# Kernel optimization log

Measured on AMD Instinct MI355X. Metric: run time of the kernel, lower is better.

The kernel has to match this reference:

```python
import jax, jax.numpy as jnp
import numpy as np

T, B, N, H, NT = 4096, 8, 256, 512, 5
W_SCALE = 0.02


def setup_inputs() -> dict:
    key = jax.random.key(0)
    ks = jax.random.split(key, 32)
    f32 = jnp.float32
    d = {}
    d['v_action'] = jax.random.normal(ks[0], (N, B, H), f32)
    d['v_frame'] = jax.random.normal(ks[1], (T, B, H), f32)
    d['v_task'] = jax.random.normal(ks[2], (NT, B, H), f32)
    d['v_mask'] = jax.random.randint(ks[3], (B, N), 0, 2, jnp.int32).at[:, 0].set(1)
    d['t_action'] = jax.random.normal(ks[4], (N, B, H), f32)
    d['t_frame'] = jax.random.normal(ks[5], (T, B, H), f32)
    d['t_task'] = jax.random.normal(ks[6], (NT, B, H), f32)
    d['t_mask'] = jax.random.randint(ks[7], (B, N), 0, 2, jnp.int32).at[:, 0].set(1)
    names = ['v_Wq', 'v_Wk', 'v_Wv', 'v_Wo', 't_Wq', 't_Wk', 't_Wv', 't_Wo']
    for i, nm in enumerate(names):
        d[nm] = jax.random.normal(ks[8 + i], (H, H), f32) * W_SCALE
    d['v_aw'] = jnp.asarray(0.1, f32)
    d['t_aw'] = jnp.asarray(0.1, f32)
    d['v_tw'] = jax.random.normal(ks[20], (H, 1), f32) * W_SCALE
    d['v_tb'] = jnp.zeros((1,), f32)
    d['t_tw'] = jax.random.normal(ks[21], (H, 1), f32) * W_SCALE
    d['t_tb'] = jnp.zeros((1,), f32)
    return d


def _compute_logit(frame, action, Wq, Wk):
    # frame: [T,B,H] queries, action: [N,B,H] keys -> logits [B,T,N]
    q = jnp.einsum('tbf,fh->tbh', frame, Wq)
    k = jnp.einsum('nba,ah->nbh', action, Wk)
    return jnp.einsum('tbh,nbh->btn', q, k) / jnp.sqrt(jnp.asarray(q.shape[-1], q.dtype))


def _compute_output(logit, alignment, action, frame, mask, Wv, Wo, aw):
    # shared detached cross-domain alignment, gated by sigmoid(alignment_weight)
    combined = logit + jax.nn.sigmoid(aw) * alignment          # [B,T,N]
    nomask = combined
    masked = jnp.where(mask[:, None, :] > 0, combined, -jnp.inf)
    attn = jax.nn.softmax(masked, axis=-1)                      # softmax over protos N
    v = jnp.einsum('nba,af->nbf', action, Wv)                   # values from protos
    out = jnp.einsum('btn,nbf->tbf', attn, v)
    out = jnp.einsum('tbf,fg->tbg', out, Wo) + frame            # residual to frames
    return out, nomask


def reference(v_action, v_frame, v_task, v_mask, t_action, t_frame, t_task, t_mask,
              v_Wq, v_Wk, v_Wv, v_Wo, v_aw, v_tw, v_tb,
              t_Wq, t_Wk, t_Wv, t_Wo, t_aw, t_tw, t_tb):
    v_logit = _compute_logit(v_frame, v_action, v_Wq, v_Wk)
    t_logit = _compute_logit(t_frame, t_action, t_Wq, t_Wk)
    v_share = jax.lax.stop_gradient(v_logit)
    t_share = jax.lax.stop_gradient(t_logit)
    v_out, v_nm = _compute_output(v_logit, t_share, v_action, v_frame, v_mask, v_Wv, v_Wo, v_aw)
    t_out, t_nm = _compute_output(t_logit, v_share, t_action, t_frame, t_mask, t_Wv, t_Wo, t_aw)
    v_ta = jnp.einsum('kbh,ho->kbo', v_task, v_tw) + v_tb       # [ntask,B,1]
    t_ta = jnp.einsum('kbh,ho->kbo', t_task, t_tw) + t_tb
    return (v_out, t_out,
            jnp.transpose(v_nm, (0, 2, 1)),                      # [B,N,T]
            jnp.transpose(t_nm, (0, 2, 1)),
            v_ta, t_ta)
```

## Files before the change

kernel.cpp:

```cpp
#include <hip/hip_runtime.h>
#include <hip/hip_bf16.h>
#include <cstddef>
#include <cstdint>

#define T_DIM 4096
#define B_DIM 8
#define N_DIM 256
#define H_DIM 512
#define NT_DIM 5

typedef __attribute__((ext_vector_type(8))) short short8;
typedef __attribute__((ext_vector_type(4))) float f32x4;

__device__ __forceinline__ short cvt_bf16(float f) {
  __hip_bfloat16 h = __float2bfloat16(f);
  union { __hip_bfloat16 h; short s; } u; u.h = h; return u.s;
}
__device__ __forceinline__ float bf2f(short s) {
  union { uint32_t u; float f; } v; v.u = ((uint32_t)(uint16_t)s) << 16;
  return v.f;
}

typedef __attribute__((address_space(1))) const void gvoid_t;
typedef __attribute__((address_space(3))) void lvoid_t;
__device__ __forceinline__ void gl_lds16(const void* g, void* lds_wave_base) {
  __builtin_amdgcn_global_load_lds((gvoid_t*)(uintptr_t)g,
                                   (lvoid_t*)(uint32_t)(uintptr_t)lds_wave_base,
                                   16, 0, 0);
}

struct GP {
  const void* A[2];
  const short* B[2];
  void* C[2];
  const float* R[2];
};

template<typename TA, typename TC, bool ADD_RES>
__global__ __launch_bounds__(256)
void gemm_tn(GP p, int zlog, long long a_bs, int lda,
             long long b_bs, int ldb, long long c_bs, int ldc,
             int K, float scale) {
  constexpr bool F32A = (sizeof(TA) == 4);
  constexpr int ASTR = F32A ? 40 : 32;
  constexpr int AB = 128 * ASTR * 2;
  constexpr int BB = 128 * 32 * 2;
  constexpr int HALF = AB + BB;
  constexpr int EPIB = 4 * 16 * 68 * 4;
  constexpr int SMEMB = (2 * HALF) > EPIB ? (2 * HALF) : EPIB;
  __shared__ __align__(16) char smem[SMEMB];

  const int tid  = threadIdx.x;
  const int lane = tid & 63;
  const int wave = tid >> 6;
  const int wr   = (wave >> 1) * 64;
  const int wc   = (wave & 1) * 64;
  const int lrow = lane & 15;
  const int kgrp = lane >> 4;

  const int dom = blockIdx.z >> zlog;
  const long long zz = blockIdx.z & ((1u << zlog) - 1u);

  const TA*    Abase = (const TA*)p.A[dom] + zz * a_bs + (long long)(blockIdx.x * 128) * lda;
  const short* Bbase = p.B[dom] + zz * b_bs + (long long)(blockIdx.y * 128) * ldb;

  const int ch_r  = lane >> 2;
  const int swcol = ((lane & 3) ^ (ch_r & 3)) * 8;
  const int srow = tid >> 1;
  const int scol = (tid & 1) * 16;

  f32x4 acc[4][4] = {};
  f32x4 pv[4];

  auto stageA_bf16 = [&](int bufoff, int k0) {
    short* As = (short*)(smem + bufoff);
    #pragma unroll
    for (int i = 0; i < 2; ++i) {
      const int c = wave + 4 * i;
      gl_lds16((const short*)Abase + (long long)(c * 16 + ch_r) * lda + k0 + swcol,
               &As[c * 512]);
    }
  };
  auto stageB = [&](int bufoff, int k0) {
    short* Bs = (short*)(smem + bufoff + AB);
    #pragma unroll
    for (int i = 0; i < 2; ++i) {
      const int c = wave + 4 * i;
      gl_lds16(Bbase + (long long)(c * 16 + ch_r) * ldb + k0 + swcol, &Bs[c * 512]);
    }
  };
  auto loadA_f32 = [&](int k0) {
    const float* gp = (const float*)Abase + (long long)srow * lda + k0 + scol;
    pv[0] = *(const f32x4*)(gp + 0);
    pv[1] = *(const f32x4*)(gp + 4);
    pv[2] = *(const f32x4*)(gp + 8);
    pv[3] = *(const f32x4*)(gp + 12);
  };
  auto writeA_f32 = [&](int bufoff) {
    short* As = (short*)(smem + bufoff);
    short8 s0, s1;
    #pragma unroll
    for (int e = 0; e < 4; ++e) {
      s0[e]     = cvt_bf16(pv[0][e]);
      s0[4 + e] = cvt_bf16(pv[1][e]);
      s1[e]     = cvt_bf16(pv[2][e]);
      s1[4 + e] = cvt_bf16(pv[3][e]);
    }
    *(short8*)&As[srow * ASTR + scol]     = s0;
    *(short8*)&As[srow * ASTR + scol + 8] = s1;
  };
  auto compute = [&](int bufoff) {
    short* As = (short*)(smem + bufoff);
    short* Bs = (short*)(smem + bufoff + AB);
    short8 af[4], bfr[4];
    const int u = kgrp ^ (lrow & 3);
    #pragma unroll
    for (int i = 0; i < 4; ++i) {
      const int row = wr + i * 16 + lrow;
      if constexpr (F32A) af[i] = *(const short8*)&As[row * ASTR + kgrp * 8];
      else                af[i] = *(const short8*)&As[row * 32 + u * 8];
    }
    #pragma unroll
    for (int j = 0; j < 4; ++j) {
      const int row = wc + j * 16 + lrow;
      bfr[j] = *(const short8*)&Bs[row * 32 + u * 8];
    }
    #pragma unroll
    for (int i = 0; i < 4; ++i)
      #pragma unroll
      for (int j = 0; j < 4; ++j)
        acc[i][j] = __builtin_amdgcn_mfma_f32_16x16x32_bf16(af[i], bfr[j], acc[i][j], 0, 0, 0);
  };

  const int NT = K >> 5;
  if constexpr (F32A) {
    loadA_f32(0); writeA_f32(0); stageB(0, 0);
    __syncthreads();
    int cur = 0;
    for (int t = 0; t < NT; ++t) {
      const int nxt = (cur ^ 1) * HALF;
      const bool more = (t + 1 < NT);
      if (more) { loadA_f32((t + 1) << 5); stageB(nxt, (t + 1) << 5); }
      compute(cur * HALF);
      if (more) writeA_f32(nxt);
      __syncthreads();
      cur ^= 1;
    }
  } else {
    stageA_bf16(0, 0); stageB(0, 0);
    for (int t = 0; t < NT; ++t) {
      const int cb_ = (t & 1) * HALF;
      const int nb_ = ((t + 1) & 1) * HALF;
      __builtin_amdgcn_s_barrier();
      if (t + 1 < NT) { stageA_bf16(nb_, (t + 1) << 5); stageB(nb_, (t + 1) << 5); }
      __builtin_amdgcn_sched_barrier(0);
      if (t + 1 < NT) asm volatile("s_waitcnt vmcnt(4)" ::: "memory");
      else            asm volatile("s_waitcnt vmcnt(0)" ::: "memory");
      __builtin_amdgcn_sched_barrier(0);
      __builtin_amdgcn_s_barrier();
      __builtin_amdgcn_sched_barrier(0);
      compute(cb_);
    }
  }

  __syncthreads();
  float* myEp = (float*)smem + wave * (16 * 68);
  TC* Cd = (TC*)p.C[dom];
  const float* Res = p.R[dom];
  const long long cb = zz * c_bs;
  const int gm = blockIdx.x * 128 + wr;
  const int gn = blockIdx.y * 128 + wc;
  const int er = lane >> 2;
  const int ec = (lane & 3) * 16;

  f32x4 resA[4], resB[4];
  if constexpr (ADD_RES) {
    const long long b0 = cb + (long long)(gm + er) * ldc + gn + ec;
    #pragma unroll
    for (int q = 0; q < 4; ++q) resA[q] = *(const f32x4*)&Res[b0 + q * 4];
  }

  #pragma unroll
  for (int i = 0; i < 4; ++i) {
    if constexpr (ADD_RES) {
      if (i < 3) {
        const long long bn = cb + (long long)(gm + (i + 1) * 16 + er) * ldc + gn + ec;
        #pragma unroll
        for (int q = 0; q < 4; ++q) resB[q] = *(const f32x4*)&Res[bn + q * 4];
      }
    }
    #pragma unroll
    for (int j = 0; j < 4; ++j)
      #pragma unroll
      for (int r = 0; r < 4; ++r)
        myEp[(kgrp * 4 + r) * 68 + j * 16 + lrow] = acc[i][j][r];
    float vals[16];
    #pragma unroll
    for (int q = 0; q < 4; ++q) {
      f32x4 t4 = *(const f32x4*)&myEp[er * 68 + ec + q * 4];
      vals[q * 4 + 0] = t4[0]; vals[q * 4 + 1] = t4[1];
      vals[q * 4 + 2] = t4[2]; vals[q * 4 + 3] = t4[3];
    }
    const int row_g = gm + i * 16 + er;
    const long long base = cb + (long long)row_g * ldc + gn + ec;
    if constexpr (sizeof(TC) == 2) {
      short8 s0, s1;
      #pragma unroll
      for (int e = 0; e < 8; ++e) {
        s0[e] = cvt_bf16(vals[e] * scale);
        s1[e] = cvt_bf16(vals[8 + e] * scale);
      }
      *(short8*)&Cd[base]     = s0;
      *(short8*)&Cd[base + 8] = s1;
    } else {
      #pragma unroll
      for (int q = 0; q < 4; ++q) {
        f32x4 o;
        #pragma unroll
        for (int e = 0; e < 4; ++e) o[e] = vals[q * 4 + e] * scale;
        if constexpr (ADD_RES) {
          #pragma unroll
          for (int e = 0; e < 4; ++e) o[e] += resA[q][e];
        }
        *(f32x4*)&Cd[base + q * 4] = o;
      }
    }
    if constexpr (ADD_RES) {
      #pragma unroll
      for (int q = 0; q < 4; ++q) resA[q] = resB[q];
    }
  }
}

struct WSrc { const float* p[8]; };

__global__ __launch_bounds__(256)
void wtrans_kernel(WSrc s, short* __restrict__ dst) {
  __shared__ float tile[32][33];
  const int w = blockIdx.z;
  const float* src = s.p[w];
  short* d = dst + (long long)w * H_DIM * H_DIM;
  const int tx = threadIdx.x, ty = threadIdx.y;
  const int n0 = blockIdx.x * 32, k0 = blockIdx.y * 32;
  #pragma unroll
  for (int i = 0; i < 4; ++i)
    tile[ty + 8 * i][tx] = src[(long long)(k0 + ty + 8 * i) * H_DIM + n0 + tx];
  __syncthreads();
  #pragma unroll
  for (int i = 0; i < 4; ++i)
    d[(long long)(n0 + ty + 8 * i) * H_DIM + k0 + tx] = cvt_bf16(tile[tx][ty + 8 * i]);
}

__global__ __launch_bounds__(256)
void softmax_fused(const short* __restrict__ Lv, const short* __restrict__ Lt,
                   const int* __restrict__ vmask, const int* __restrict__ tmask,
                   const float* __restrict__ vaw, const float* __restrict__ taw,
                   short* __restrict__ Av, short* __restrict__ At,
                   float* __restrict__ Onm_v, float* __restrict__ Onm_t) {
  __shared__ float tile[16 * 260];
  __shared__ int msk[2][256];
  const int tid = threadIdx.x;
  const int b = blockIdx.y, t0 = blockIdx.x * 16;
  const int r = tid >> 4, seg = tid & 15;
  msk[0][tid] = vmask[b * 256 + tid];
  msk[1][tid] = tmask[b * 256 + tid];
  __syncthreads();
  const float sv = 1.f / (1.f + __expf(-vaw[0]));
  const float st = 1.f / (1.f + __expf(-taw[0]));
  const long long off = ((long long)b * T_DIM + t0 + r) * N_DIM + seg * 16;

  short8 lv0 = *(const short8*)&Lv[off];
  short8 lv1 = *(const short8*)&Lv[off + 8];
  short8 lt0 = *(const short8*)&Lt[off];
  short8 lt1 = *(const short8*)&Lt[off + 8];
  float cv[16], ct[16];
  #pragma unroll
  for (int i = 0; i < 8; ++i) {
    float a0 = bf2f(lv0[i]), b0 = bf2f(lt0[i]);
    float a1 = bf2f(lv1[i]), b1 = bf2f(lt1[i]);
    cv[i]     = a0 + sv * b0;  ct[i]     = b0 + st * a0;
    cv[8 + i] = a1 + sv * b1;  ct[8 + i] = b1 + st * a1;
  }

#define EMIT_DOMAIN(CVAL, DI, AOUT, ONM) do {                                   \
    const int4 mA = *(const int4*)&msk[DI][seg * 16 + 0];                       \
    const int4 mB = *(const int4*)&msk[DI][seg * 16 + 4];                       \
    const int4 mC = *(const int4*)&msk[DI][seg * 16 + 8];                       \
    const int4 mD = *(const int4*)&msk[DI][seg * 16 + 12];                      \
    const int mk[16] = {mA.x, mA.y, mA.z, mA.w, mB.x, mB.y, mB.z, mB.w,         \
                        mC.x, mC.y, mC.z, mC.w, mD.x, mD.y, mD.z, mD.w};        \
    float mx = -3.4e38f;                                                        \
    _Pragma("unroll")                                                           \
    for (int q = 0; q < 16; ++q) if (mk[q] > 0) mx = fmaxf(mx, CVAL[q]);        \
    _Pragma("unroll")                                                           \
    for (int sh = 1; sh < 16; sh <<= 1) mx = fmaxf(mx, __shfl_xor(mx, sh));     \
    float ev[16]; float ssum = 0.f;                                             \
    _Pragma("unroll")                                                           \
    for (int q = 0; q < 16; ++q) {                                              \
      ev[q] = (mk[q] > 0) ? __expf(CVAL[q] - mx) : 0.f; ssum += ev[q];          \
    }                                                                           \
    _Pragma("unroll")                                                           \
    for (int sh = 1; sh < 16; sh <<= 1) ssum += __shfl_xor(ssum, sh);           \
    const float inv = 1.f / ssum;                                               \
    short8 o0, o1;                                                              \
    _Pragma("unroll")                                                           \
    for (int q = 0; q < 8; ++q) {                                               \
      o0[q] = cvt_bf16(ev[q] * inv); o1[q] = cvt_bf16(ev[8 + q] * inv);         \
    }                                                                           \
    *(short8*)&AOUT[off] = o0; *(short8*)&AOUT[off + 8] = o1;                   \
    _Pragma("unroll")                                                           \
    for (int q = 0; q < 4; ++q) {                                               \
      f32x4 tv; tv[0] = CVAL[q * 4]; tv[1] = CVAL[q * 4 + 1];                   \
      tv[2] = CVAL[q * 4 + 2]; tv[3] = CVAL[q * 4 + 3];                         \
      *(f32x4*)&tile[r * 260 + seg * 16 + q * 4] = tv;                          \
    }                                                                           \
    __syncthreads();                                                            \
    {                                                                           \
      float* obase = &ONM[((long long)b * N_DIM + tid) * T_DIM + t0];           \
      _Pragma("unroll")                                                         \
      for (int g = 0; g < 4; ++g) {                                             \
        f32x4 wv;                                                               \
        wv[0] = tile[(4 * g + 0) * 260 + tid];                                  \
        wv[1] = tile[(4 * g + 1) * 260 + tid];                                  \
        wv[2] = tile[(4 * g + 2) * 260 + tid];                                  \
        wv[3] = tile[(4 * g + 3) * 260 + tid];                                  \
        *(f32x4*)&obase[4 * g] = wv;                                            \
      }                                                                         \
    }                                                                           \
    __syncthreads();                                                            \
  } while (0)

  EMIT_DOMAIN(cv, 0, Av, Onm_v);
  EMIT_DOMAIN(ct, 1, At, Onm_t);
#undef EMIT_DOMAIN
}

__global__ __launch_bounds__(1024)
void task_kernel(const float* __restrict__ vtask, const float* __restrict__ ttask,
                 const float* __restrict__ vtw, const float* __restrict__ vtb,
                 const float* __restrict__ ttw, const float* __restrict__ ttb,
                 float* __restrict__ out_v, float* __restrict__ out_t) {
  const int wave = threadIdx.x >> 6;
  const int lane = threadIdx.x & 63;
  const int dom = wave >> 3;
  const int b   = wave & 7;
  const float* task = dom ? ttask : vtask;
  const float* tw   = dom ? ttw : vtw;
  const float  tb   = (dom ? ttb : vtb)[0];
  float* o = dom ? out_t : out_v;
  for (int k = 0; k < NT_DIM; ++k) {
    const float* row = task + ((long long)k * B_DIM + b) * H_DIM;
    float s = 0.f;
    for (int c = lane; c < H_DIM; c += 64) s += row[c] * tw[c];
    #pragma unroll
    for (int d = 32; d > 0; d >>= 1) s += __shfl_xor(s, d);
    if (lane == 0) o[k * B_DIM + b] = s + tb;
  }
}

extern "C" void kernel_launch(void* const* d_in, const int* in_sizes, int n_in,
                              void* d_out, int out_size, void* d_ws, size_t ws_size,
                              hipStream_t stream) {
  const float* v_action = (const float*)d_in[0];
  const float* v_frame  = (const float*)d_in[1];
  const float* v_task   = (const float*)d_in[2];
  const int*   v_mask   = (const int*)d_in[3];
  const float* t_action = (const float*)d_in[4];
  const float* t_frame  = (const float*)d_in[5];
  const float* t_task   = (const float*)d_in[6];
  const int*   t_mask   = (const int*)d_in[7];
  const float* v_aw = (const float*)d_in[16];
  const float* t_aw = (const float*)d_in[17];
  const float* v_tw = (const float*)d_in[18];
  const float* v_tb = (const float*)d_in[19];
  const float* t_tw = (const float*)d_in[20];
  const float* t_tb = (const float*)d_in[21];

  const long long TBH = (long long)T_DIM * B_DIM * H_DIM;
  const long long BTN = (long long)B_DIM * T_DIM * N_DIM;
  const long long NBH = (long long)N_DIM * B_DIM * H_DIM;
  const long long WS  = (long long)H_DIM * H_DIM;

  float* out = (float*)d_out;
  float* out_v   = out;
  float* out_t   = out + TBH;
  float* out_vnm = out + 2 * TBH;
  float* out_tnm = out + 2 * TBH + BTN;
  float* out_vta = out + 2 * TBH + 2 * BTN;
  float* out_tta = out_vta + NT_DIM * B_DIM;

  char* w = (char*)d_ws;
  auto alloc = [&](long long bytes) {
    char* p = w; w += (bytes + 255) & ~255LL; return p;
  };
  short* WT   = (short*)alloc(8 * WS * 2);
  short* Qv   = (short*)alloc(TBH * 2);
  short* Qt   = (short*)alloc(TBH * 2);
  short* KVv  = (short*)alloc(2048LL * 1024 * 2);
  short* KVt  = (short*)alloc(2048LL * 1024 * 2);
  short* VWTv = (short*)alloc(NBH * 2);
  short* VWTt = (short*)alloc(NBH * 2);
  short* Av   = (short*)alloc(BTN * 2);
  short* At   = (short*)alloc(BTN * 2);
  short* Lv   = (short*)alloc(BTN * 2);
  short* Lt   = (short*)alloc(BTN * 2);

  const float rsq = 0.044194173824159216f;

  WSrc ws8;
  for (int i = 0; i < 8; ++i) ws8.p[i] = (const float*)d_in[8 + i];
  wtrans_kernel<<<dim3(16, 16, 8), dim3(32, 8), 0, stream>>>(ws8, WT);

  {
    GP p = {{v_frame, t_frame}, {WT + 0 * WS, WT + 4 * WS}, {Qv, Qt}, {nullptr, nullptr}};
    gemm_tn<float, short, false><<<dim3(256, 4, 2), dim3(256), 0, stream>>>(
        p, 0, 0LL, H_DIM, 0LL, H_DIM, 0LL, H_DIM, 512, 1.f);
  }

  {
    GP p = {{v_action, t_action}, {WT + 1 * WS, WT + 5 * WS}, {KVv, KVt}, {nullptr, nullptr}};
    gemm_tn<float, short, false><<<dim3(16, 8, 2), dim3(256), 0, stream>>>(
        p, 0, 0LL, H_DIM, 0LL, H_DIM, 0LL, 1024, 512, 1.f);
  }

  {
    GP p = {{WT + 3 * WS, WT + 7 * WS}, {KVv + 512, KVt + 512}, {VWTv, VWTt},
            {nullptr, nullptr}};
    gemm_tn<short, short, false><<<dim3(4, 2, 16), dim3(256), 0, stream>>>(
        p, 3, 0LL, H_DIM, 1024LL, 8192, (long long)H_DIM * N_DIM, N_DIM, 512, 1.f);
  }

  {
    GP p = {{Qv, Qt}, {KVv, KVt}, {Lv, Lt}, {nullptr, nullptr}};
    gemm_tn<short, short, false><<<dim3(32, 2, 16), dim3(256), 0, stream>>>(
        p, 3, 512LL, B_DIM * H_DIM, 1024LL, 8192,
        (long long)T_DIM * N_DIM, N_DIM, 512, rsq);
  }

  softmax_fused<<<dim3(T_DIM / 16, B_DIM), dim3(256), 0, stream>>>(
      Lv, Lt, v_mask, t_mask, v_aw, t_aw, Av, At, out_vnm, out_tnm);

  {
    GP p = {{Av, At}, {VWTv, VWTt}, {out_v, out_t}, {v_frame, t_frame}};
    gemm_tn<short, float, true><<<dim3(32, 4, 16), dim3(256), 0, stream>>>(
        p, 3, (long long)T_DIM * N_DIM, N_DIM, (long long)H_DIM * N_DIM, N_DIM,
        512LL, B_DIM * H_DIM, 256, 1.f);
  }

  task_kernel<<<dim3(1), dim3(1024), 0, stream>>>(
      v_task, t_task, v_tw, v_tb, t_tw, t_tb, out_vta, out_tta);
}
```

Before: 292.3 us.

## Fuse logits GEMM with cross-domain softmax and triple-buffer bf16 GEMM loads

The QK logits GEMM for both domains now runs inside a new kernel that keeps logits in registers, mixes them across domains, applies the masked softmax, and writes the bf16 attention weights and the fp32 transposed logits directly. This removes the bf16 logits round-trip through global memory and one kernel launch. It also keeps the logits in fp32 before mixing instead of rounding them to bf16. Separately, the bf16 path of the generic GEMM moves from double to triple buffering with a deeper prefetch distance. The cost is a large LDS footprint (144KB per block) and many block-wide syncs in the epilogue, which limits occupancy.

```diff
diff --git a/kernel.cpp b/kernel.cpp
--- a/kernel.cpp
+++ b/kernel.cpp
@@ -15,10 +15,6 @@
 __device__ __forceinline__ short cvt_bf16(float f) {
   __hip_bfloat16 h = __float2bfloat16(f);
   union { __hip_bfloat16 h; short s; } u; u.h = h; return u.s;
-}
-__device__ __forceinline__ float bf2f(short s) {
-  union { uint32_t u; float f; } v; v.u = ((uint32_t)(uint16_t)s) << 16;
-  return v.f;
 }
 
 typedef __attribute__((address_space(1))) const void gvoid_t;
@@ -28,6 +24,8 @@
                                    (lvoid_t*)(uint32_t)(uintptr_t)lds_wave_base,
                                    16, 0, 0);
 }
+
+#define MFMA16(a, b, c) __builtin_amdgcn_mfma_f32_16x16x32_bf16(a, b, c, 0, 0, 0)
 
 struct GP {
   const void* A[2];
@@ -46,8 +44,9 @@
   constexpr int AB = 128 * ASTR * 2;
   constexpr int BB = 128 * 32 * 2;
   constexpr int HALF = AB + BB;
+  constexpr int NBUF = F32A ? 2 : 3;
   constexpr int EPIB = 4 * 16 * 68 * 4;
-  constexpr int SMEMB = (2 * HALF) > EPIB ? (2 * HALF) : EPIB;
+  constexpr int SMEMB = (NBUF * HALF) > EPIB ? (NBUF * HALF) : EPIB;
   __shared__ __align__(16) char smem[SMEMB];
 
   const int tid  = threadIdx.x;
@@ -129,7 +128,7 @@
     for (int i = 0; i < 4; ++i)
       #pragma unroll
       for (int j = 0; j < 4; ++j)
-        acc[i][j] = __builtin_amdgcn_mfma_f32_16x16x32_bf16(af[i], bfr[j], acc[i][j], 0, 0, 0);
+        acc[i][j] = MFMA16(af[i], bfr[j], acc[i][j]);
   };
 
   const int NT = K >> 5;
@@ -148,14 +147,20 @@
     }
   } else {
     stageA_bf16(0, 0); stageB(0, 0);
+    stageA_bf16(HALF, 32); stageB(HALF, 32);
     for (int t = 0; t < NT; ++t) {
-      const int cb_ = (t & 1) * HALF;
-      const int nb_ = ((t + 1) & 1) * HALF;
+      const int cb_ = (t % 3) * HALF;
       __builtin_amdgcn_s_barrier();
-      if (t + 1 < NT) { stageA_bf16(nb_, (t + 1) << 5); stageB(nb_, (t + 1) << 5); }
-      __builtin_amdgcn_sched_barrier(0);
-      if (t + 1 < NT) asm volatile("s_waitcnt vmcnt(4)" ::: "memory");
-      else            asm volatile("s_waitcnt vmcnt(0)" ::: "memory");
+      if (t + 2 < NT) {
+        const int nb_ = ((t + 2) % 3) * HALF;
+        stageA_bf16(nb_, (t + 2) << 5); stageB(nb_, (t + 2) << 5);
+        __builtin_amdgcn_sched_barrier(0);
+        asm volatile("s_waitcnt vmcnt(8)" ::: "memory");
+      } else if (t + 1 < NT) {
+        asm volatile("s_waitcnt vmcnt(4)" ::: "memory");
+      } else {
+        asm volatile("s_waitcnt vmcnt(0)" ::: "memory");
+      }
       __builtin_amdgcn_sched_barrier(0);
       __builtin_amdgcn_s_barrier();
       __builtin_amdgcn_sched_barrier(0);
@@ -230,6 +235,201 @@
       for (int q = 0; q < 4; ++q) resA[q] = resB[q];
     }
   }
+}
+
+__global__ __launch_bounds__(512)
+void logits_softmax_fused(const short* __restrict__ Qvg, const short* __restrict__ Qtg,
+                          const short* __restrict__ KVv, const short* __restrict__ KVt,
+                          const int* __restrict__ vmask, const int* __restrict__ tmask,
+                          const float* __restrict__ vaw, const float* __restrict__ taw,
+                          short* __restrict__ Avg, short* __restrict__ Atg,
+                          float* __restrict__ Onm_v, float* __restrict__ Onm_t) {
+  constexpr int TILEB = 48 * 1024;
+  __shared__ __align__(16) char smem[3 * TILEB];
+  __shared__ float rowstat[128][4];
+
+  const int tid  = threadIdx.x;
+  const int lane = tid & 63;
+  const int wave = tid >> 6;
+  const int wm   = wave >> 2;
+  const int wn   = wave & 3;
+  const int lrow = lane & 15;
+  const int kgrp = lane >> 4;
+  const int b    = blockIdx.y;
+  const int t0   = blockIdx.x * 128;
+
+  const float sv = 1.f / (1.f + __expf(-vaw[0]));
+  const float st = 1.f / (1.f + __expf(-taw[0]));
+  const float rsq = 0.044194173824159216f;
+
+  int mkv[4], mkt[4];
+  #pragma unroll
+  for (int j = 0; j < 4; ++j) {
+    const int n = wn * 64 + j * 16 + lrow;
+    mkv[j] = vmask[b * 256 + n];
+    mkt[j] = tmask[b * 256 + n];
+  }
+
+  const int ch_r = lane >> 2;
+  const int sw8  = ((lane & 3) ^ (ch_r & 3)) * 8;
+  const short* gsrc[6];
+  int loff[6];
+  #pragma unroll
+  for (int i = 0; i < 6; ++i) {
+    const int c = wave * 6 + i;
+    const short* s;
+    if (c < 8)       s = Qvg + (long long)(t0 + c * 16 + ch_r) * 4096 + b * 512;
+    else if (c < 16) s = Qtg + (long long)(t0 + (c - 8) * 16 + ch_r) * 4096 + b * 512;
+    else if (c < 32) s = KVv + (long long)((c - 16) * 16 + ch_r) * 8192 + b * 1024;
+    else             s = KVt + (long long)((c - 32) * 16 + ch_r) * 8192 + b * 1024;
+    gsrc[i] = s + sw8;
+    loff[i] = c * 1024;
+  }
+  auto stage = [&](int buf, int k0) {
+    #pragma unroll
+    for (int i = 0; i < 6; ++i)
+      gl_lds16(gsrc[i] + k0, smem + buf * TILEB + loff[i]);
+  };
+
+  f32x4 accv[4][4] = {}, acct[4][4] = {};
+
+  auto compute = [&](int buf) {
+    const short* L = (const short*)(smem + buf * TILEB);
+    const int u = kgrp ^ (lrow & 3);
+    short8 qv[4], qt[4], kv[4], kt[4];
+    #pragma unroll
+    for (int i = 0; i < 4; ++i) {
+      const int r = wm * 64 + i * 16 + lrow;
+      qv[i] = *(const short8*)&L[r * 32 + u * 8];
+      qt[i] = *(const short8*)&L[4096 + r * 32 + u * 8];
+    }
+    #pragma unroll
+    for (int j = 0; j < 4; ++j) {
+      const int r = wn * 64 + j * 16 + lrow;
+      kv[j] = *(const short8*)&L[8192 + r * 32 + u * 8];
+      kt[j] = *(const short8*)&L[16384 + r * 32 + u * 8];
+    }
+    #pragma unroll
+    for (int i = 0; i < 4; ++i)
+      #pragma unroll
+      for (int j = 0; j < 4; ++j) {
+        accv[i][j] = MFMA16(qv[i], kv[j], accv[i][j]);
+        acct[i][j] = MFMA16(qt[i], kt[j], acct[i][j]);
+      }
+  };
+
+  stage(0, 0); stage(1, 32);
+  #pragma unroll 1
+  for (int t = 0; t < 16; ++t) {
+    __builtin_amdgcn_s_barrier();
+    if (t + 2 < 16) {
+      stage((t + 2) % 3, (t + 2) * 32);
+      __builtin_amdgcn_sched_barrier(0);
+      asm volatile("s_waitcnt vmcnt(12)" ::: "memory");
+    } else if (t + 1 < 16) {
+      asm volatile("s_waitcnt vmcnt(6)" ::: "memory");
+    } else {
+      asm volatile("s_waitcnt vmcnt(0)" ::: "memory");
+    }
+    __builtin_amdgcn_sched_barrier(0);
+    __builtin_amdgcn_s_barrier();
+    __builtin_amdgcn_sched_barrier(0);
+    compute(t % 3);
+  }
+  __syncthreads();
+
+  #pragma unroll
+  for (int i = 0; i < 4; ++i)
+    #pragma unroll
+    for (int j = 0; j < 4; ++j) {
+      f32x4 a = accv[i][j], c = acct[i][j];
+      #pragma unroll
+      for (int e = 0; e < 4; ++e) {
+        accv[i][j][e] = rsq * (a[e] + sv * c[e]);
+        acct[i][j][e] = rsq * (c[e] + st * a[e]);
+      }
+    }
+
+#define DOM_OUT(ACC, MK, AV_G, ONM_G) do {                                          \
+    float lm[4][4];                                                                 \
+    _Pragma("unroll") for (int i = 0; i < 4; ++i)                                   \
+    _Pragma("unroll") for (int r = 0; r < 4; ++r) {                                 \
+      float m = -3.4e38f;                                                           \
+      _Pragma("unroll") for (int j = 0; j < 4; ++j)                                 \
+        if (MK[j] > 0) m = fmaxf(m, ACC[i][j][r]);                                  \
+      m = fmaxf(m, __shfl_xor(m, 1)); m = fmaxf(m, __shfl_xor(m, 2));               \
+      m = fmaxf(m, __shfl_xor(m, 4)); m = fmaxf(m, __shfl_xor(m, 8));               \
+      lm[i][r] = m;                                                                 \
+    }                                                                               \
+    if (lrow == 0) {                                                                \
+      _Pragma("unroll") for (int i = 0; i < 4; ++i)                                 \
+      _Pragma("unroll") for (int r = 0; r < 4; ++r)                                 \
+        rowstat[wm * 64 + i * 16 + kgrp * 4 + r][wn] = lm[i][r];                    \
+    }                                                                               \
+    __syncthreads();                                                                \
+    _Pragma("unroll") for (int i = 0; i < 4; ++i)                                   \
+    _Pragma("unroll") for (int r = 0; r < 4; ++r) {                                 \
+      f32x4 s = *(const f32x4*)&rowstat[wm * 64 + i * 16 + kgrp * 4 + r][0];        \
+      lm[i][r] = fmaxf(fmaxf(s[0], s[1]), fmaxf(s[2], s[3]));                       \
+    }                                                                               \
+    __syncthreads();                                                                \
+    float ls[4][4];                                                                 \
+    _Pragma("unroll") for (int i = 0; i < 4; ++i)                                   \
+    _Pragma("unroll") for (int r = 0; r < 4; ++r) {                                 \
+      float s = 0.f;                                                                \
+      _Pragma("unroll") for (int j = 0; j < 4; ++j)                                 \
+        if (MK[j] > 0) s += __expf(ACC[i][j][r] - lm[i][r]);                        \
+      s += __shfl_xor(s, 1); s += __shfl_xor(s, 2);                                 \
+      s += __shfl_xor(s, 4); s += __shfl_xor(s, 8);                                 \
+      ls[i][r] = s;                                                                 \
+    }                                                                               \
+    if (lrow == 0) {                                                                \
+      _Pragma("unroll") for (int i = 0; i < 4; ++i)                                 \
+      _Pragma("unroll") for (int r = 0; r < 4; ++r)                                 \
+        rowstat[wm * 64 + i * 16 + kgrp * 4 + r][wn] = ls[i][r];                    \
+    }                                                                               \
+    __syncthreads();                                                                \
+    _Pragma("unroll") for (int i = 0; i < 4; ++i)                                   \
+    _Pragma("unroll") for (int r = 0; r < 4; ++r) {                                 \
+      f32x4 s = *(const f32x4*)&rowstat[wm * 64 + i * 16 + kgrp * 4 + r][0];        \
+      ls[i][r] = 1.f / (s[0] + s[1] + s[2] + s[3]);                                 \
+    }                                                                               \
+    __syncthreads();                                                                \
+    {                    \
+      short* AL = (short*)smem;                                                     \
+      _Pragma("unroll") for (int i = 0; i < 4; ++i)                                 \
+      _Pragma("unroll") for (int j = 0; j < 4; ++j)                                 \
+      _Pragma("unroll") for (int r = 0; r < 4; ++r) {                               \
+        float e = (MK[j] > 0) ? __expf(ACC[i][j][r] - lm[i][r]) * ls[i][r] : 0.f;   \
+        AL[(wm * 64 + i * 16 + kgrp * 4 + r) * 264 + wn * 64 + j * 16 + lrow] =     \
+            cvt_bf16(e);                                                            \
+      }                                                                             \
+      __syncthreads();                                                              \
+      const int rr = tid >> 2, cb0 = (tid & 3) * 64;                                \
+      short* dst = AV_G + ((long long)b * T_DIM + t0 + rr) * 256 + cb0;             \
+      _Pragma("unroll") for (int q = 0; q < 8; ++q)                                 \
+        *(short8*)&dst[q * 8] = *(const short8*)&AL[rr * 264 + cb0 + q * 8];        \
+      __syncthreads();                                                              \
+    }                                                                               \
+    {                \
+      float* OL = (float*)smem;                                                     \
+      _Pragma("unroll") for (int i = 0; i < 4; ++i)                                 \
+      _Pragma("unroll") for (int j = 0; j < 4; ++j)                                 \
+      _Pragma("unroll") for (int r = 0; r < 4; ++r)                                 \
+        OL[(wn * 64 + j * 16 + lrow) * 132 + wm * 64 + i * 16 + kgrp * 4 + r] =     \
+            ACC[i][j][r];                                                           \
+      __syncthreads();                                                              \
+      const int nn = tid >> 1, c0 = (tid & 1) * 64;                                 \
+      float* dst = ONM_G + ((long long)b * 256 + nn) * T_DIM + t0 + c0;             \
+      _Pragma("unroll") for (int q = 0; q < 16; ++q)                                \
+        *(f32x4*)&dst[q * 4] = *(const f32x4*)&OL[nn * 132 + c0 + q * 4];           \
+      __syncthreads();                                                              \
+    }                                                                               \
+  } while (0)
+
+  DOM_OUT(accv, mkv, Avg, Onm_v);
+  DOM_OUT(acct, mkt, Atg, Onm_t);
+#undef DOM_OUT
 }
 
 struct WSrc { const float* p[8]; };
@@ -249,90 +449,6 @@
   #pragma unroll
   for (int i = 0; i < 4; ++i)
     d[(long long)(n0 + ty + 8 * i) * H_DIM + k0 + tx] = cvt_bf16(tile[tx][ty + 8 * i]);
-}
-
-__global__ __launch_bounds__(256)
-void softmax_fused(const short* __restrict__ Lv, const short* __restrict__ Lt,
-                   const int* __restrict__ vmask, const int* __restrict__ tmask,
-                   const float* __restrict__ vaw, const float* __restrict__ taw,
-                   short* __restrict__ Av, short* __restrict__ At,
-                   float* __restrict__ Onm_v, float* __restrict__ Onm_t) {
-  __shared__ float tile[16 * 260];
-  __shared__ int msk[2][256];
-  const int tid = threadIdx.x;
-  const int b = blockIdx.y, t0 = blockIdx.x * 16;
-  const int r = tid >> 4, seg = tid & 15;
-  msk[0][tid] = vmask[b * 256 + tid];
-  msk[1][tid] = tmask[b * 256 + tid];
-  __syncthreads();
-  const float sv = 1.f / (1.f + __expf(-vaw[0]));
-  const float st = 1.f / (1.f + __expf(-taw[0]));
-  const long long off = ((long long)b * T_DIM + t0 + r) * N_DIM + seg * 16;
-
-  short8 lv0 = *(const short8*)&Lv[off];
-  short8 lv1 = *(const short8*)&Lv[off + 8];
-  short8 lt0 = *(const short8*)&Lt[off];
-  short8 lt1 = *(const short8*)&Lt[off + 8];
-  float cv[16], ct[16];
-  #pragma unroll
-  for (int i = 0; i < 8; ++i) {
-    float a0 = bf2f(lv0[i]), b0 = bf2f(lt0[i]);
-    float a1 = bf2f(lv1[i]), b1 = bf2f(lt1[i]);
-    cv[i]     = a0 + sv * b0;  ct[i]     = b0 + st * a0;
-    cv[8 + i] = a1 + sv * b1;  ct[8 + i] = b1 + st * a1;
-  }
-
-#define EMIT_DOMAIN(CVAL, DI, AOUT, ONM) do {                                   \
-    const int4 mA = *(const int4*)&msk[DI][seg * 16 + 0];                       \
-    const int4 mB = *(const int4*)&msk[DI][seg * 16 + 4];                       \
-    const int4 mC = *(const int4*)&msk[DI][seg * 16 + 8];                       \
-    const int4 mD = *(const int4*)&msk[DI][seg * 16 + 12];                      \
-    const int mk[16] = {mA.x, mA.y, mA.z, mA.w, mB.x, mB.y, mB.z, mB.w,         \
-                        mC.x, mC.y, mC.z, mC.w, mD.x, mD.y, mD.z, mD.w};        \
-    float mx = -3.4e38f;                                                        \
-    _Pragma("unroll")                                                           \
-    for (int q = 0; q < 16; ++q) if (mk[q] > 0) mx = fmaxf(mx, CVAL[q]);        \
-    _Pragma("unroll")                                                           \
-    for (int sh = 1; sh < 16; sh <<= 1) mx = fmaxf(mx, __shfl_xor(mx, sh));     \
-    float ev[16]; float ssum = 0.f;                                             \
-    _Pragma("unroll")                                                           \
-    for (int q = 0; q < 16; ++q) {                                              \
-      ev[q] = (mk[q] > 0) ? __expf(CVAL[q] - mx) : 0.f; ssum += ev[q];          \
-    }                                                                           \
-    _Pragma("unroll")                                                           \
-    for (int sh = 1; sh < 16; sh <<= 1) ssum += __shfl_xor(ssum, sh);           \
-    const float inv = 1.f / ssum;                                               \
-    short8 o0, o1;                                                              \
-    _Pragma("unroll")                                                           \
-    for (int q = 0; q < 8; ++q) {                                               \
-      o0[q] = cvt_bf16(ev[q] * inv); o1[q] = cvt_bf16(ev[8 + q] * inv);         \
-    }                                                                           \
-    *(short8*)&AOUT[off] = o0; *(short8*)&AOUT[off + 8] = o1;                   \
-    _Pragma("unroll")                                                           \
-    for (int q = 0; q < 4; ++q) {                                               \
-      f32x4 tv; tv[0] = CVAL[q * 4]; tv[1] = CVAL[q * 4 + 1];                   \
-      tv[2] = CVAL[q * 4 + 2]; tv[3] = CVAL[q * 4 + 3];                         \
-      *(f32x4*)&tile[r * 260 + seg * 16 + q * 4] = tv;                          \
-    }                                                                           \
-    __syncthreads();                                                            \
-    {                                                                           \
-      float* obase = &ONM[((long long)b * N_DIM + tid) * T_DIM + t0];           \
-      _Pragma("unroll")                                                         \
-      for (int g = 0; g < 4; ++g) {                                             \
-        f32x4 wv;                                                               \
-        wv[0] = tile[(4 * g + 0) * 260 + tid];                                  \
-        wv[1] = tile[(4 * g + 1) * 260 + tid];                                  \
-        wv[2] = tile[(4 * g + 2) * 260 + tid];                                  \
-        wv[3] = tile[(4 * g + 3) * 260 + tid];                                  \
-        *(f32x4*)&obase[4 * g] = wv;                                            \
-      }                                                                         \
-    }                                                                           \
-    __syncthreads();                                                            \
-  } while (0)
-
-  EMIT_DOMAIN(cv, 0, Av, Onm_v);
-  EMIT_DOMAIN(ct, 1, At, Onm_t);
-#undef EMIT_DOMAIN
 }
 
 __global__ __launch_bounds__(1024)
@@ -402,10 +518,6 @@
   short* VWTt = (short*)alloc(NBH * 2);
   short* Av   = (short*)alloc(BTN * 2);
   short* At   = (short*)alloc(BTN * 2);
-  short* Lv   = (short*)alloc(BTN * 2);
-  short* Lt   = (short*)alloc(BTN * 2);
-
-  const float rsq = 0.044194173824159216f;
 
   WSrc ws8;
   for (int i = 0; i < 8; ++i) ws8.p[i] = (const float*)d_in[8 + i];
@@ -430,15 +542,8 @@
         p, 3, 0LL, H_DIM, 1024LL, 8192, (long long)H_DIM * N_DIM, N_DIM, 512, 1.f);
   }
 
-  {
-    GP p = {{Qv, Qt}, {KVv, KVt}, {Lv, Lt}, {nullptr, nullptr}};
-    gemm_tn<short, short, false><<<dim3(32, 2, 16), dim3(256), 0, stream>>>(
-        p, 3, 512LL, B_DIM * H_DIM, 1024LL, 8192,
-        (long long)T_DIM * N_DIM, N_DIM, 512, rsq);
-  }
-
-  softmax_fused<<<dim3(T_DIM / 16, B_DIM), dim3(256), 0, stream>>>(
-      Lv, Lt, v_mask, t_mask, v_aw, t_aw, Av, At, out_vnm, out_tnm);
+  logits_softmax_fused<<<dim3(T_DIM / 128, B_DIM), dim3(512), 0, stream>>>(
+      Qv, Qt, KVv, KVt, v_mask, t_mask, v_aw, t_aw, Av, At, out_vnm, out_tnm);
 
   {
     GP p = {{Av, At}, {VWTv, VWTt}, {out_v, out_t}, {v_frame, t_frame}};
```

Result: slower. 312.8 us (+7.0%).

## Deepen GEMM K-loop pipeline to triple-buffered LDS with prefetch distance two

Applied to the files above, without the earlier changes.

Both GEMM variants now keep three LDS stages so async global-to-LDS loads run two K-tiles ahead of compute, with explicit vmcnt waits sized to the extra loads in flight. The f32-A path keeps A double-buffered through registers but triple-buffers B, and replaces __syncthreads with manual waitcnt and barrier pairs. The aim is to hide global memory latency better in the K loop. In exchange the kernel uses more LDS, which can lower occupancy, and hand-tuned vmcnt counts risk subtle ordering bugs.

```diff
diff --git a/kernel.cpp b/kernel.cpp
--- a/kernel.cpp
+++ b/kernel.cpp
@@ -28,6 +28,8 @@
                                    (lvoid_t*)(uint32_t)(uintptr_t)lds_wave_base,
                                    16, 0, 0);
 }
+
+#define MFMA16(a, b, c) __builtin_amdgcn_mfma_f32_16x16x32_bf16(a, b, c, 0, 0, 0)
 
 struct GP {
   const void* A[2];
@@ -47,7 +49,8 @@
   constexpr int BB = 128 * 32 * 2;
   constexpr int HALF = AB + BB;
   constexpr int EPIB = 4 * 16 * 68 * 4;
-  constexpr int SMEMB = (2 * HALF) > EPIB ? (2 * HALF) : EPIB;
+  constexpr int BODYB = F32A ? (2 * AB + 3 * BB) : (3 * HALF);
+  constexpr int SMEMB = BODYB > EPIB ? BODYB : EPIB;
   __shared__ __align__(16) char smem[SMEMB];
 
   const int tid  = threadIdx.x;
@@ -72,8 +75,8 @@
   f32x4 acc[4][4] = {};
   f32x4 pv[4];
 
-  auto stageA_bf16 = [&](int bufoff, int k0) {
-    short* As = (short*)(smem + bufoff);
+  auto stageA_bf16 = [&](int buf, int k0) {
+    short* As = (short*)(smem + buf * HALF);
     #pragma unroll
     for (int i = 0; i < 2; ++i) {
       const int c = wave + 4 * i;
@@ -81,8 +84,16 @@
                &As[c * 512]);
     }
   };
-  auto stageB = [&](int bufoff, int k0) {
-    short* Bs = (short*)(smem + bufoff + AB);
+  auto stageB_bf16 = [&](int buf, int k0) {
+    short* Bs = (short*)(smem + buf * HALF + AB);
+    #pragma unroll
+    for (int i = 0; i < 2; ++i) {
+      const int c = wave + 4 * i;
+      gl_lds16(Bbase + (long long)(c * 16 + ch_r) * ldb + k0 + swcol, &Bs[c * 512]);
+    }
+  };
+  auto stageB_f32p = [&](int buf, int k0) {
+    short* Bs = (short*)(smem + 2 * AB + buf * BB);
     #pragma unroll
     for (int i = 0; i < 2; ++i) {
       const int c = wave + 4 * i;
@@ -96,8 +107,8 @@
     pv[2] = *(const f32x4*)(gp + 8);
     pv[3] = *(const f32x4*)(gp + 12);
   };
-  auto writeA_f32 = [&](int bufoff) {
-    short* As = (short*)(smem + bufoff);
+  auto writeA_f32 = [&](int buf) {
+    short* As = (short*)(smem + buf * AB);
     short8 s0, s1;
     #pragma unroll
     for (int e = 0; e < 4; ++e) {
@@ -109,9 +120,10 @@
     *(short8*)&As[srow * ASTR + scol]     = s0;
     *(short8*)&As[srow * ASTR + scol + 8] = s1;
   };
-  auto compute = [&](int bufoff) {
-    short* As = (short*)(smem + bufoff);
-    short* Bs = (short*)(smem + bufoff + AB);
+  auto compute = [&](int abuf, int bbuf) {
+    const short* As = (const short*)(smem + (F32A ? abuf * AB : abuf * HALF));
+    const short* Bs = (const short*)(smem + (F32A ? 2 * AB + bbuf * BB
+                                                  : bbuf * HALF + AB));
     short8 af[4], bfr[4];
     const int u = kgrp ^ (lrow & 3);
     #pragma unroll
@@ -129,37 +141,50 @@
     for (int i = 0; i < 4; ++i)
       #pragma unroll
       for (int j = 0; j < 4; ++j)
-        acc[i][j] = __builtin_amdgcn_mfma_f32_16x16x32_bf16(af[i], bfr[j], acc[i][j], 0, 0, 0);
+        acc[i][j] = MFMA16(af[i], bfr[j], acc[i][j]);
   };
 
   const int NT = K >> 5;
   if constexpr (F32A) {
-    loadA_f32(0); writeA_f32(0); stageB(0, 0);
-    __syncthreads();
-    int cur = 0;
+    loadA_f32(0); writeA_f32(0);
+    stageB_f32p(0, 0);
+    if (NT > 1) stageB_f32p(1, 32);
+    if (NT > 1) loadA_f32(32);
     for (int t = 0; t < NT; ++t) {
-      const int nxt = (cur ^ 1) * HALF;
-      const bool more = (t + 1 < NT);
-      if (more) { loadA_f32((t + 1) << 5); stageB(nxt, (t + 1) << 5); }
-      compute(cur * HALF);
-      if (more) writeA_f32(nxt);
-      __syncthreads();
-      cur ^= 1;
+      asm volatile("s_waitcnt lgkmcnt(0)" ::: "memory");
+      __builtin_amdgcn_sched_barrier(0);
+      __builtin_amdgcn_s_barrier();
+      if (t + 2 < NT) stageB_f32p((t + 2) % 3, (t + 2) << 5);
+      __builtin_amdgcn_sched_barrier(0);
+      if (t + 2 < NT)      asm volatile("s_waitcnt vmcnt(8)" ::: "memory");
+      else if (t + 1 < NT) asm volatile("s_waitcnt vmcnt(6)" ::: "memory");
+      else                 asm volatile("s_waitcnt vmcnt(0)" ::: "memory");
+      __builtin_amdgcn_sched_barrier(0);
+      __builtin_amdgcn_s_barrier();
+      __builtin_amdgcn_sched_barrier(0);
+      compute(t & 1, t % 3);
+      if (t + 1 < NT) writeA_f32((t + 1) & 1);
+      if (t + 2 < NT) loadA_f32((t + 2) << 5);
     }
   } else {
-    stageA_bf16(0, 0); stageB(0, 0);
+    stageA_bf16(0, 0); stageB_bf16(0, 0);
+    if (NT > 1) { stageA_bf16(1, 32); stageB_bf16(1, 32); }
     for (int t = 0; t < NT; ++t) {
-      const int cb_ = (t & 1) * HALF;
-      const int nb_ = ((t + 1) & 1) * HALF;
       __builtin_amdgcn_s_barrier();
-      if (t + 1 < NT) { stageA_bf16(nb_, (t + 1) << 5); stageB(nb_, (t + 1) << 5); }
-      __builtin_amdgcn_sched_barrier(0);
-      if (t + 1 < NT) asm volatile("s_waitcnt vmcnt(4)" ::: "memory");
-      else            asm volatile("s_waitcnt vmcnt(0)" ::: "memory");
+      if (t + 2 < NT) {
+        stageA_bf16((t + 2) % 3, (t + 2) << 5);
+        stageB_bf16((t + 2) % 3, (t + 2) << 5);
+        __builtin_amdgcn_sched_barrier(0);
+        asm volatile("s_waitcnt vmcnt(8)" ::: "memory");
+      } else if (t + 1 < NT) {
+        asm volatile("s_waitcnt vmcnt(4)" ::: "memory");
+      } else {
+        asm volatile("s_waitcnt vmcnt(0)" ::: "memory");
+      }
       __builtin_amdgcn_sched_barrier(0);
       __builtin_amdgcn_s_barrier();
       __builtin_amdgcn_sched_barrier(0);
-      compute(cb_);
+      compute(t % 3, t % 3);
     }
   }
 
```

Result: no change. 290.3 us (-0.7%).
